# Performance work log

Measured on AMD Instinct MI355X. Metric: run time of the kernel, lower is better.

Reference implementation:

```python
import jax, jax.numpy as jnp
import numpy as np

B, S, D, H = 2, 4096, 512, 8
HD = D // H


def setup_inputs() -> dict:
    key = jax.random.key(0)
    ks = jax.random.split(key, 11)
    s = 1.0 / np.sqrt(D)
    return {
        "queries": jax.random.normal(ks[0], (B, S, D), jnp.float32),
        "keys": jax.random.normal(ks[1], (B, S, D), jnp.float32),
        "values": jax.random.normal(ks[2], (B, S, D), jnp.float32),
        "Wq": jax.random.normal(ks[3], (D, D), jnp.float32) * s,
        "bq": jnp.zeros((D,), jnp.float32),
        "Wk": jax.random.normal(ks[4], (D, D), jnp.float32) * s,
        "bk": jnp.zeros((D,), jnp.float32),
        "Wv": jax.random.normal(ks[5], (D, D), jnp.float32) * s,
        "bv": jnp.zeros((D,), jnp.float32),
        "Wo": jax.random.normal(ks[6], (D, D), jnp.float32) * s,
        "bo": jnp.zeros((D,), jnp.float32),
    }


def reference(queries, keys, values, Wq, bq, Wk, bk, Wv, bv, Wo, bo):
    b = queries.shape[0]
    # Linear projections (torch Linear: x @ W.T + b; here W stored as [in, out])
    q = (queries @ Wq + bq).reshape(b, -1, H, HD)   # [B, Sq, H, HD]
    k = (keys @ Wk + bk).reshape(b, -1, H, HD)       # [B, Sk, H, HD]
    v = (values @ Wv + bv).reshape(b, -1, H, HD)     # [B, Sk, H, HD]
    logits = jnp.einsum('bqhd,bkhd->bhqk', q, k) / jnp.sqrt(jnp.float32(HD))
    attn = jax.nn.softmax(logits, axis=-1)           # [B, H, Sq, Sk]  (dropout_rate=0 -> identity)
    ctx = jnp.einsum('bhqk,bkhd->bqhd', attn, v).reshape(b, -1, H * HD)
    return ctx @ Wo + bo
```

## Files before the change

### kernel.cpp

```cpp
#include <hip/hip_runtime.h>
#include <hip/hip_bf16.h>

constexpr int B_  = 2;
constexpr int S_  = 4096;
constexpr int D_  = 512;
constexpr int H_  = 8;
constexpr int HD_ = 64;
constexpr int M_  = B_ * S_;

typedef __attribute__((ext_vector_type(8))) short short8;
typedef __attribute__((ext_vector_type(4))) float floatx4;

static __device__ __forceinline__ unsigned short f2bf(float f) {
    union { float f; unsigned u; } v; v.f = f;
    unsigned r = v.u + 0x7fffu + ((v.u >> 16) & 1u);
    return (unsigned short)(r >> 16);
}

static __device__ __forceinline__ unsigned pk2bf(float a, float b) {
#if __has_builtin(__builtin_amdgcn_cvt_pk_bf16_f32)
    typedef __attribute__((ext_vector_type(2))) __bf16 bf16x2_t;
    union { bf16x2_t v; unsigned u; } u;
    u.v = __builtin_amdgcn_cvt_pk_bf16_f32(a, b);
    return u.u;
#else
    return (unsigned)f2bf(a) | ((unsigned)f2bf(b) << 16);
#endif
}

#if __has_builtin(__builtin_amdgcn_exp2f)
#define EXP2(x) __builtin_amdgcn_exp2f(x)
#else
#define EXP2(x) exp2f(x)
#endif

#define QSCALE 0.18033688011110204f

static __device__ __forceinline__ void gl_lds16(const void* g, void* l) {
    typedef __attribute__((address_space(1))) const unsigned GU;
    typedef __attribute__((address_space(3))) unsigned LU;
    __builtin_amdgcn_global_load_lds((GU*)g, (LU*)l, 16, 0, 0);
}

__global__ __launch_bounds__(256) void xcast_kernel(
    const float* __restrict__ Xq, const float* __restrict__ Xk, const float* __restrict__ Xv,
    unsigned short* __restrict__ Y) {
    const int z = blockIdx.z;
    const float* X = z == 0 ? Xq : (z == 1 ? Xk : Xv);
    unsigned short* Yz = Y + (size_t)z * M_ * D_;
    const int n8 = M_ * D_ / 8;
    int i = blockIdx.x * 256 + threadIdx.x;
    const int stride = gridDim.x * 256;
    for (; i < n8; i += stride) {
        float4 a = *(const float4*)&X[(size_t)i * 8];
        float4 b = *(const float4*)&X[(size_t)i * 8 + 4];
        union { short8 s; unsigned u[4]; } p;
        p.u[0] = pk2bf(a.x, a.y); p.u[1] = pk2bf(a.z, a.w);
        p.u[2] = pk2bf(b.x, b.y); p.u[3] = pk2bf(b.z, b.w);
        *(short8*)&Yz[(size_t)i * 8] = p.s;
    }
}

__global__ __launch_bounds__(256) void wtrans_kernel(
    const float* __restrict__ Wq, const float* __restrict__ Wk,
    const float* __restrict__ Wv, const float* __restrict__ Wo,
    unsigned short* __restrict__ Tq, unsigned short* __restrict__ Tk,
    unsigned short* __restrict__ Tv, unsigned short* __restrict__ To) {
    const int z = blockIdx.z;
    const float* W = z == 0 ? Wq : (z == 1 ? Wk : (z == 2 ? Wv : Wo));
    unsigned short* Wt = z == 0 ? Tq : (z == 1 ? Tk : (z == 2 ? Tv : To));
    __shared__ float T[64][65];
    const int t = threadIdx.x;
    const int k0 = blockIdx.x * 64, n0 = blockIdx.y * 64;
#pragma unroll
    for (int i = 0; i < 4; ++i) {
        const int flat = t + 256 * i;
        const int kr = flat >> 4, nc = (flat & 15) * 4;
        float4 v = *(const float4*)&W[(size_t)(k0 + kr) * 512 + n0 + nc];
        T[kr][nc] = v.x; T[kr][nc + 1] = v.y; T[kr][nc + 2] = v.z; T[kr][nc + 3] = v.w;
    }
    __syncthreads();
#pragma unroll
    for (int i = 0; i < 4; ++i) {
        const int flat = t + 256 * i;
        const int nr = flat >> 4, kc = (flat & 15) * 4;
        ushort4 o4;
        o4.x = f2bf(T[kc][nr]);     o4.y = f2bf(T[kc + 1][nr]);
        o4.z = f2bf(T[kc + 2][nr]); o4.w = f2bf(T[kc + 3][nr]);
        *(ushort4*)&Wt[(size_t)(n0 + nr) * 512 + k0 + kc] = o4;
    }
}

template <int MODE>
__global__ __launch_bounds__(256, 3) void gemm_kernel(
    const unsigned short* __restrict__ Ab,
    const unsigned short* __restrict__ Wt,
    const float* __restrict__ b0, const float* __restrict__ b1, const float* __restrict__ b2,
    unsigned short* __restrict__ o0, unsigned short* __restrict__ o1,
    unsigned short* __restrict__ o2, float* __restrict__ of) {
    __shared__ unsigned short As[128 * 64];
    __shared__ unsigned short Bs[128 * 64];

    const int tid  = threadIdx.x;
    const int w    = tid >> 6;
    const int lane = tid & 63;
    const int n0   = blockIdx.x * 128;
    const int m0   = blockIdx.y * 128;
    const int lm   = lane & 15;
    const int lq   = lane >> 4;
    const int wm   = (w >> 1) * 64;
    const int wn   = (w & 1) * 64;

    const int z = MODE == 0 ? (n0 >> 9) : 0;
    const unsigned short* A = MODE == 0 ? Ab + (size_t)z * M_ * D_ : Ab;

    const int srow = lane >> 3;
    const int sch  = lane & 7;
    const int ca   = (sch ^ (srow & 7)) * 8;

    floatx4 acc[4][4];
#pragma unroll
    for (int i = 0; i < 4; ++i)
#pragma unroll
        for (int j = 0; j < 4; ++j) acc[i][j] = (floatx4)0.0f;

    for (int kb = 0; kb < 8; ++kb) {
        const int k0 = kb * 64;
        __syncthreads();
#pragma unroll
        for (int it = 0; it < 4; ++it) {
            const int r8 = w * 32 + it * 8;
            gl_lds16(&A [(size_t)(m0 + r8 + srow) * 512 + k0 + ca], &As[r8 * 64]);
            gl_lds16(&Wt[(size_t)(n0 + r8 + srow) * 512 + k0 + ca], &Bs[r8 * 64]);
        }
        __syncthreads();

        short8 af[2][4], bf[2][4];
#pragma unroll
        for (int ks = 0; ks < 2; ++ks)
#pragma unroll
            for (int i = 0; i < 4; ++i) {
                const int cc = ((ks * 4 + lq) ^ (lm & 7)) * 8;
                af[ks][i] = *(const short8*)&As[(wm + i * 16 + lm) * 64 + cc];
                bf[ks][i] = *(const short8*)&Bs[(wn + i * 16 + lm) * 64 + cc];
            }
#pragma unroll
        for (int ks = 0; ks < 2; ++ks)
#pragma unroll
            for (int mi = 0; mi < 4; ++mi)
#pragma unroll
                for (int ni = 0; ni < 4; ++ni)
                    acc[mi][ni] = __builtin_amdgcn_mfma_f32_16x16x32_bf16(
                        af[ks][mi], bf[ks][ni], acc[mi][ni], 0, 0, 0);
    }

    const float* bias = MODE == 0 ? (z == 0 ? b0 : (z == 1 ? b1 : b2)) : b0;
    const float scale = (MODE == 0 && z == 0) ? QSCALE : 1.0f;
    const int nl0 = n0 & 511;

    float bias_n[4];
#pragma unroll
    for (int ni = 0; ni < 4; ++ni) bias_n[ni] = bias[nl0 + wn + ni * 16 + lm];

#pragma unroll
    for (int mi = 0; mi < 4; ++mi) {
#pragma unroll
        for (int ni = 0; ni < 4; ++ni) {
            if (MODE == 1) {
                const int gn = n0 + wn + ni * 16 + lm;
#pragma unroll
                for (int r = 0; r < 4; ++r) {
                    const int gm = m0 + wm + mi * 16 + lq * 4 + r;
                    of[(size_t)gm * 512 + gn] = acc[mi][ni][r] + bias_n[ni];
                }
            } else {
                const int gnl = nl0 + wn + ni * 16 + lm;
                const int h = gnl >> 6, hd = gnl & 63;
                if (z == 2) {
                    const int gm = m0 + wm + mi * 16 + lq * 4;
                    const int b = gm >> 12, s = gm & 4095;
                    union { ushort4 s4; uint2 u; } o4;
                    o4.u.x = pk2bf(acc[mi][ni][0] + bias_n[ni], acc[mi][ni][1] + bias_n[ni]);
                    o4.u.y = pk2bf(acc[mi][ni][2] + bias_n[ni], acc[mi][ni][3] + bias_n[ni]);
                    *(ushort4*)&o2[(((size_t)(b * 8 + h)) * 64 + hd) * 4096 + s] = o4.s4;
                } else {
                    unsigned short* out = z == 0 ? o0 : o1;
#pragma unroll
                    for (int r = 0; r < 4; ++r) {
                        const int gm = m0 + wm + mi * 16 + lq * 4 + r;
                        const int b = gm >> 12, s = gm & 4095;
                        const float vv = (acc[mi][ni][r] + bias_n[ni]) * scale;
                        out[(((size_t)(b * 8 + h)) * 4096 + s) * 64 + hd] = f2bf(vv);
                    }
                }
            }
        }
    }
}

__global__ __launch_bounds__(256, 2) void flash_kernel(
    const unsigned short* __restrict__ Q, const unsigned short* __restrict__ K,
    const unsigned short* __restrict__ Vt, unsigned short* __restrict__ ctx) {
    __shared__ unsigned short Ks[64 * 64];
    __shared__ unsigned short Vs[64 * 64];
    __shared__ unsigned short Ps[4][16 * 64];

    const int tid = threadIdx.x;
    const int w   = tid >> 6;
    const int l   = tid & 63;
    const int lm  = l & 15;
    const int lq  = l >> 4;
    const int q0  = blockIdx.x * 128;
    const int bh  = blockIdx.y;

    const size_t base = (size_t)bh * S_ * HD_;
    const unsigned short* Qg = Q + base;
    const unsigned short* Kg = K + base;
    const unsigned short* Vg = Vt + base;

    short8 qf[2][2];
#pragma unroll
    for (int qn = 0; qn < 2; ++qn) {
        const unsigned short* qp = &Qg[(size_t)(q0 + w * 32 + qn * 16 + lm) * 64];
        qf[qn][0] = *(const short8*)(qp + lq * 8);
        qf[qn][1] = *(const short8*)(qp + 32 + lq * 8);
    }

    short8 ones;
#pragma unroll
    for (int j = 0; j < 8; ++j) ones[j] = (short)0x3F80;

    floatx4 o[2][4];
#pragma unroll
    for (int qn = 0; qn < 2; ++qn)
#pragma unroll
        for (int i = 0; i < 4; ++i) o[qn][i] = (floatx4)0.0f;
    floatx4 ls[2];
    ls[0] = (floatx4)0.0f; ls[1] = (floatx4)0.0f;

    const int sr  = tid >> 3, sch = tid & 7;
    const int sw0 = sr * 64 + ((sch ^ (sr & 7)) * 8);
    const int sw1 = (sr + 32) * 64 + ((sch ^ (sr & 7)) * 8);
    const int lm7 = lm & 7;

    short8 kr0, kr1, vr0, vr1;
    kr0 = *(const short8*)&Kg[(size_t)sr * 64 + sch * 8];
    kr1 = *(const short8*)&Kg[(size_t)(sr + 32) * 64 + sch * 8];
    vr0 = *(const short8*)&Vg[(size_t)sr * S_ + sch * 8];
    vr1 = *(const short8*)&Vg[(size_t)(sr + 32) * S_ + sch * 8];

    for (int kt = 0; kt < 64; ++kt) {
        __syncthreads();
        *(short8*)&Ks[sw0] = kr0;
        *(short8*)&Ks[sw1] = kr1;
        *(short8*)&Vs[sw0] = vr0;
        *(short8*)&Vs[sw1] = vr1;
        __syncthreads();
        if (kt < 63) {
            const int t1 = (kt + 1) * 64;
            kr0 = *(const short8*)&Kg[(size_t)(t1 + sr) * 64 + sch * 8];
            kr1 = *(const short8*)&Kg[(size_t)(t1 + sr + 32) * 64 + sch * 8];
            vr0 = *(const short8*)&Vg[(size_t)sr * S_ + t1 + sch * 8];
            vr1 = *(const short8*)&Vg[(size_t)(sr + 32) * S_ + t1 + sch * 8];
        }

        short8 kf[2][4];
#pragma unroll
        for (int ks = 0; ks < 2; ++ks)
#pragma unroll
            for (int ni = 0; ni < 4; ++ni)
                kf[ks][ni] = *(const short8*)&Ks[(ni * 16 + lm) * 64 +
                                                 (((ks * 4 + lq) ^ lm7) * 8)];

        floatx4 sf[2][4];
#pragma unroll
        for (int qn = 0; qn < 2; ++qn)
#pragma unroll
            for (int ni = 0; ni < 4; ++ni) sf[qn][ni] = (floatx4)0.0f;
#pragma unroll
        for (int ks = 0; ks < 2; ++ks)
#pragma unroll
            for (int qn = 0; qn < 2; ++qn)
#pragma unroll
                for (int ni = 0; ni < 4; ++ni)
                    sf[qn][ni] = __builtin_amdgcn_mfma_f32_16x16x32_bf16(
                        kf[ks][ni], qf[qn][ks], sf[qn][ni], 0, 0, 0);

        short8 vf[2][4];
#pragma unroll
        for (int c = 0; c < 2; ++c)
#pragma unroll
            for (int ni = 0; ni < 4; ++ni)
                vf[c][ni] = *(const short8*)&Vs[(ni * 16 + lm) * 64 +
                                                (((c * 4 + lq) ^ lm7) * 8)];

        unsigned short* Pw = &Ps[w][0];
#pragma unroll
        for (int qn = 0; qn < 2; ++qn) {
#pragma unroll
            for (int ni = 0; ni < 4; ++ni) {
                uint2 pv;
                pv.x = pk2bf(EXP2(sf[qn][ni][0]), EXP2(sf[qn][ni][1]));
                pv.y = pk2bf(EXP2(sf[qn][ni][2]), EXP2(sf[qn][ni][3]));
                *(uint2*)&Pw[lm * 64 + (((ni * 2 + (lq >> 1)) ^ lm7) * 8) + (lq & 1) * 4] = pv;
            }
#pragma unroll
            for (int c = 0; c < 2; ++c) {
                short8 pf = *(const short8*)&Pw[lm * 64 + (((c * 4 + lq) ^ lm7) * 8)];
                ls[qn] = __builtin_amdgcn_mfma_f32_16x16x32_bf16(ones, pf, ls[qn], 0, 0, 0);
#pragma unroll
                for (int ni = 0; ni < 4; ++ni)
                    o[qn][ni] = __builtin_amdgcn_mfma_f32_16x16x32_bf16(
                        vf[c][ni], pf, o[qn][ni], 0, 0, 0);
            }
        }
    }

    const int b = bh >> 3, h = bh & 7;
#pragma unroll
    for (int qn = 0; qn < 2; ++qn) {
        const float inv = 1.0f / ls[qn][0];
        const int q = q0 + w * 32 + qn * 16 + lm;
        const size_t rb = ((size_t)(b * S_ + q)) * 512 + h * 64;
#pragma unroll
        for (int ni = 0; ni < 4; ++ni) {
            union { ushort4 s; uint2 u; } o4;
            o4.u.x = pk2bf(o[qn][ni][0] * inv, o[qn][ni][1] * inv);
            o4.u.y = pk2bf(o[qn][ni][2] * inv, o[qn][ni][3] * inv);
            *(ushort4*)&ctx[rb + ni * 16 + lq * 4] = o4.s;
        }
    }
}

extern "C" void kernel_launch(void* const* d_in, const int* in_sizes, int n_in,
                              void* d_out, int out_size, void* d_ws, size_t ws_size,
                              hipStream_t stream) {
    const float* queries = (const float*)d_in[0];
    const float* keys    = (const float*)d_in[1];
    const float* values  = (const float*)d_in[2];
    const float* Wq = (const float*)d_in[3];
    const float* bq = (const float*)d_in[4];
    const float* Wk = (const float*)d_in[5];
    const float* bk = (const float*)d_in[6];
    const float* Wv = (const float*)d_in[7];
    const float* bv = (const float*)d_in[8];
    const float* Wo = (const float*)d_in[9];
    const float* bo = (const float*)d_in[10];

    unsigned short* xb    = (unsigned short*)d_ws;
    unsigned short* wsctx = xb;
    unsigned short* wsq   = xb   + (size_t)3 * M_ * D_;
    unsigned short* wsk   = wsq  + (size_t)M_ * D_;
    unsigned short* wsvt  = wsk  + (size_t)M_ * D_;
    unsigned short* wtq   = wsvt + (size_t)M_ * D_;
    unsigned short* wtk   = wtq  + (size_t)D_ * D_;
    unsigned short* wtv   = wtk  + (size_t)D_ * D_;
    unsigned short* wto   = wtv  + (size_t)D_ * D_;

    xcast_kernel<<<dim3(1024, 1, 3), dim3(256), 0, stream>>>(queries, keys, values, xb);
    wtrans_kernel<<<dim3(8, 8, 4), dim3(256), 0, stream>>>(
        Wq, Wk, Wv, Wo, wtq, wtk, wtv, wto);

    gemm_kernel<0><<<dim3(12, 64), dim3(256), 0, stream>>>(
        xb, wtq, bq, bk, bv, wsq, wsk, wsvt, nullptr);

    flash_kernel<<<dim3(S_ / 128, B_ * H_), dim3(256), 0, stream>>>(wsq, wsk, wsvt, wsctx);

    gemm_kernel<1><<<dim3(4, 64), dim3(256), 0, stream>>>(
        wsctx, wto, bo, nullptr, nullptr, nullptr, nullptr, nullptr, (float*)d_out);
}
```

Baseline: 244.0 us.

## Switch flash attention to 32x32x16 MFMA and keep P in registers via permlane swap

Rebuilds the attention inner loop around 32x32x16 bf16 MFMA instead of 16x16x32. S and O tiles become 16-float accumulators, and the probability tile is repacked in registers with permlane32_swap instead of going through a per-wave LDS scratch buffer. This removes the LDS write/read round trip for P and the Ps shared allocation, and cuts the MFMA instruction count. The costs are different register pressure from the larger accumulators and a strided epilogue that writes one bf16 per lane per row.

New measurement: 239.7 us. No clear change (-1.7%).

```diff
diff --git a/kernel.cpp b/kernel.cpp
--- a/kernel.cpp
+++ b/kernel.cpp
@@ -10,6 +10,7 @@
 
 typedef __attribute__((ext_vector_type(8))) short short8;
 typedef __attribute__((ext_vector_type(4))) float floatx4;
+typedef __attribute__((ext_vector_type(16))) float floatx16;
 
 static __device__ __forceinline__ unsigned short f2bf(float f) {
     union { float f; unsigned u; } v; v.f = f;
@@ -25,6 +26,20 @@
     return u.u;
 #else
     return (unsigned)f2bf(a) | ((unsigned)f2bf(b) << 16);
+#endif
+}
+
+static __device__ __forceinline__ void plane32swap(unsigned& x, unsigned& y) {
+#if __has_builtin(__builtin_amdgcn_permlane32_swap)
+    typedef __attribute__((ext_vector_type(2))) unsigned uint2v;
+    uint2v r = __builtin_amdgcn_permlane32_swap(x, y, false, false);
+    x = r[0]; y = r[1];
+#else
+    const bool hi = (threadIdx.x & 32) != 0;
+    unsigned xs = __shfl_xor(x, 32), ys = __shfl_xor(y, 32);
+    unsigned nx = hi ? ys : x;
+    unsigned ny = hi ? y : xs;
+    x = nx; y = ny;
 #endif
 }
 
@@ -203,45 +218,39 @@
     const unsigned short* __restrict__ Vt, unsigned short* __restrict__ ctx) {
     __shared__ unsigned short Ks[64 * 64];
     __shared__ unsigned short Vs[64 * 64];
-    __shared__ unsigned short Ps[4][16 * 64];
 
     const int tid = threadIdx.x;
     const int w   = tid >> 6;
     const int l   = tid & 63;
-    const int lm  = l & 15;
-    const int lq  = l >> 4;
+    const int lo  = l & 31;
+    const int hi  = l >> 5;
+    const int lo7 = lo & 7;
     const int q0  = blockIdx.x * 128;
     const int bh  = blockIdx.y;
+    const int qw  = q0 + w * 32;
 
     const size_t base = (size_t)bh * S_ * HD_;
     const unsigned short* Qg = Q + base;
     const unsigned short* Kg = K + base;
     const unsigned short* Vg = Vt + base;
 
-    short8 qf[2][2];
-#pragma unroll
-    for (int qn = 0; qn < 2; ++qn) {
-        const unsigned short* qp = &Qg[(size_t)(q0 + w * 32 + qn * 16 + lm) * 64];
-        qf[qn][0] = *(const short8*)(qp + lq * 8);
-        qf[qn][1] = *(const short8*)(qp + 32 + lq * 8);
-    }
+    short8 qf[4];
+#pragma unroll
+    for (int ds = 0; ds < 4; ++ds)
+        qf[ds] = *(const short8*)&Qg[(size_t)(qw + lo) * 64 + ds * 16 + hi * 8];
 
     short8 ones;
 #pragma unroll
     for (int j = 0; j < 8; ++j) ones[j] = (short)0x3F80;
 
-    floatx4 o[2][4];
-#pragma unroll
-    for (int qn = 0; qn < 2; ++qn)
-#pragma unroll
-        for (int i = 0; i < 4; ++i) o[qn][i] = (floatx4)0.0f;
-    floatx4 ls[2];
-    ls[0] = (floatx4)0.0f; ls[1] = (floatx4)0.0f;
+    floatx16 o[2];
+    o[0] = (floatx16)0.0f; o[1] = (floatx16)0.0f;
+    floatx16 lacc = (floatx16)0.0f;
 
     const int sr  = tid >> 3, sch = tid & 7;
-    const int sw0 = sr * 64 + ((sch ^ (sr & 7)) * 8);
-    const int sw1 = (sr + 32) * 64 + ((sch ^ (sr & 7)) * 8);
-    const int lm7 = lm & 7;
+    const int swz = (sch ^ (sr & 7)) * 8;
+    const int sw0 = sr * 64 + swz;
+    const int sw1 = (sr + 32) * 64 + swz;
 
     short8 kr0, kr1, vr0, vr1;
     kr0 = *(const short8*)&Kg[(size_t)sr * 64 + sch * 8];
@@ -266,69 +275,64 @@
 
         short8 kf[2][4];
 #pragma unroll
-        for (int ks = 0; ks < 2; ++ks)
-#pragma unroll
-            for (int ni = 0; ni < 4; ++ni)
-                kf[ks][ni] = *(const short8*)&Ks[(ni * 16 + lm) * 64 +
-                                                 (((ks * 4 + lq) ^ lm7) * 8)];
-
-        floatx4 sf[2][4];
-#pragma unroll
-        for (int qn = 0; qn < 2; ++qn)
-#pragma unroll
-            for (int ni = 0; ni < 4; ++ni) sf[qn][ni] = (floatx4)0.0f;
-#pragma unroll
-        for (int ks = 0; ks < 2; ++ks)
-#pragma unroll
-            for (int qn = 0; qn < 2; ++qn)
-#pragma unroll
-                for (int ni = 0; ni < 4; ++ni)
-                    sf[qn][ni] = __builtin_amdgcn_mfma_f32_16x16x32_bf16(
-                        kf[ks][ni], qf[qn][ks], sf[qn][ni], 0, 0, 0);
+        for (int g = 0; g < 2; ++g)
+#pragma unroll
+            for (int ds = 0; ds < 4; ++ds)
+                kf[g][ds] = *(const short8*)&Ks[(g * 32 + lo) * 64 +
+                                                (((ds * 2 + hi) ^ lo7) * 8)];
+        floatx16 s[2];
+        s[0] = (floatx16)0.0f; s[1] = (floatx16)0.0f;
+#pragma unroll
+        for (int g = 0; g < 2; ++g)
+#pragma unroll
+            for (int ds = 0; ds < 4; ++ds)
+                s[g] = __builtin_amdgcn_mfma_f32_32x32x16_bf16(
+                    kf[g][ds], qf[ds], s[g], 0, 0, 0);
+
+        floatx16 p[2];
+#pragma unroll
+        for (int g = 0; g < 2; ++g)
+#pragma unroll
+            for (int r = 0; r < 16; ++r) p[g][r] = EXP2(s[g][r]);
+
+        short8 pa[4];
+#pragma unroll
+        for (int ks = 0; ks < 4; ++ks) {
+            const int g = ks >> 1, kk = (ks & 1) * 8;
+            unsigned wa = pk2bf(p[g][kk + 0], p[g][kk + 1]);
+            unsigned wb = pk2bf(p[g][kk + 2], p[g][kk + 3]);
+            unsigned wc = pk2bf(p[g][kk + 4], p[g][kk + 5]);
+            unsigned wd = pk2bf(p[g][kk + 6], p[g][kk + 7]);
+            plane32swap(wa, wc);
+            plane32swap(wb, wd);
+            union { short8 s8; unsigned u[4]; } pk_;
+            pk_.u[0] = wa; pk_.u[1] = wb; pk_.u[2] = wc; pk_.u[3] = wd;
+            pa[ks] = pk_.s8;
+        }
 
         short8 vf[2][4];
 #pragma unroll
-        for (int c = 0; c < 2; ++c)
-#pragma unroll
-            for (int ni = 0; ni < 4; ++ni)
-                vf[c][ni] = *(const short8*)&Vs[(ni * 16 + lm) * 64 +
-                                                (((c * 4 + lq) ^ lm7) * 8)];
-
-        unsigned short* Pw = &Ps[w][0];
-#pragma unroll
-        for (int qn = 0; qn < 2; ++qn) {
-#pragma unroll
-            for (int ni = 0; ni < 4; ++ni) {
-                uint2 pv;
-                pv.x = pk2bf(EXP2(sf[qn][ni][0]), EXP2(sf[qn][ni][1]));
-                pv.y = pk2bf(EXP2(sf[qn][ni][2]), EXP2(sf[qn][ni][3]));
-                *(uint2*)&Pw[lm * 64 + (((ni * 2 + (lq >> 1)) ^ lm7) * 8) + (lq & 1) * 4] = pv;
-            }
-#pragma unroll
-            for (int c = 0; c < 2; ++c) {
-                short8 pf = *(const short8*)&Pw[lm * 64 + (((c * 4 + lq) ^ lm7) * 8)];
-                ls[qn] = __builtin_amdgcn_mfma_f32_16x16x32_bf16(ones, pf, ls[qn], 0, 0, 0);
-#pragma unroll
-                for (int ni = 0; ni < 4; ++ni)
-                    o[qn][ni] = __builtin_amdgcn_mfma_f32_16x16x32_bf16(
-                        vf[c][ni], pf, o[qn][ni], 0, 0, 0);
-            }
+        for (int onn = 0; onn < 2; ++onn)
+#pragma unroll
+            for (int ks = 0; ks < 4; ++ks)
+                vf[onn][ks] = *(const short8*)&Vs[(onn * 32 + lo) * 64 +
+                                                  (((ks * 2 + hi) ^ lo7) * 8)];
+#pragma unroll
+        for (int ks = 0; ks < 4; ++ks) {
+            lacc = __builtin_amdgcn_mfma_f32_32x32x16_bf16(pa[ks], ones, lacc, 0, 0, 0);
+            o[0] = __builtin_amdgcn_mfma_f32_32x32x16_bf16(pa[ks], vf[0][ks], o[0], 0, 0, 0);
+            o[1] = __builtin_amdgcn_mfma_f32_32x32x16_bf16(pa[ks], vf[1][ks], o[1], 0, 0, 0);
         }
     }
 
     const int b = bh >> 3, h = bh & 7;
 #pragma unroll
-    for (int qn = 0; qn < 2; ++qn) {
-        const float inv = 1.0f / ls[qn][0];
-        const int q = q0 + w * 32 + qn * 16 + lm;
-        const size_t rb = ((size_t)(b * S_ + q)) * 512 + h * 64;
-#pragma unroll
-        for (int ni = 0; ni < 4; ++ni) {
-            union { ushort4 s; uint2 u; } o4;
-            o4.u.x = pk2bf(o[qn][ni][0] * inv, o[qn][ni][1] * inv);
-            o4.u.y = pk2bf(o[qn][ni][2] * inv, o[qn][ni][3] * inv);
-            *(ushort4*)&ctx[rb + ni * 16 + lq * 4] = o4.s;
-        }
+    for (int r = 0; r < 16; ++r) {
+        const float inv = 1.0f / lacc[r];
+        const int q = qw + (r & 3) + 8 * (r >> 2) + 4 * hi;
+        unsigned short* cp = &ctx[((size_t)(b * S_ + q)) * 512 + h * 64 + lo];
+        cp[0]  = f2bf(o[0][r] * inv);
+        cp[32] = f2bf(o[1][r] * inv);
     }
 }
 
```
